# Kernel optimization log

Hardware: AMD Instinct MI355X
Metric: run time of the kernel (lower is better)

Reference implementation:

```python
import jax, jax.numpy as jnp
import numpy as np

DEPTH = 6

def sparsemax(z):
    # sparsemax over last axis (Martins & Astudillo 2016)
    z_sorted = -jnp.sort(-z, axis=-1)
    z_cum = jnp.cumsum(z_sorted, axis=-1)
    k = jnp.arange(1, z.shape[-1] + 1, dtype=z.dtype)
    support = k * z_sorted > z_cum - 1.0
    k_sup = jnp.sum(support, axis=-1, keepdims=True).astype(jnp.int32)
    tau_sum = jnp.take_along_axis(z_cum, k_sup - 1, axis=-1)
    tau = (tau_sum - 1.0) / k_sup.astype(z.dtype)
    return jnp.maximum(z - tau, 0.0)

def sparsemoid(x):
    return jnp.clip(0.5 * x + 0.5, 0.0, 1.0)

def make_bin_codes(depth):
    indices = jnp.arange(2 ** depth)
    offsets = 2 ** jnp.arange(depth)
    bin_codes = ((indices[None, :] // offsets[:, None]) % 2).astype(jnp.float32)
    return jnp.stack([bin_codes, 1.0 - bin_codes], axis=-1)  # [depth, 2^depth, 2]

def odste_forward(x, fsl, esl, thr, lt, resp, codes):
    # x: [B,J,D]; fsl: [n,t,J]; esl: [n,t,J,D]; thr/lt: [n,t]; resp: [n,c,D,2^t]
    fs = sparsemax(fsl)                               # [n,t,J]
    es = sparsemax(esl)                               # [n,t,J,D]
    sel = jnp.einsum('bjd,ntj->bntd', x, fs)          # feature selection
    sel = sel * jnp.sum(es, axis=2)[None]             # einsum 'bntd,ntjd->bntd'
    tl = (sel - thr[None, :, :, None]) * jnp.exp(-lt)[None, :, :, None]
    tl = jnp.stack([-tl, tl], axis=-1)                # [b,n,t,d,2]
    bins = sparsemoid(tl)
    bm = jnp.einsum('bntds,tcs->bntdc', bins, codes)  # [b,n,t,d,c]
    rw = jnp.prod(bm, axis=2)                         # [b,n,d,c]
    return jnp.einsum('bnds,ncds->bnd', rw, resp)     # [b,n,d]


def setup_inputs() -> dict:
    key = jax.random.key(0)
    B, D, n, t, c_tree = 64, 32, 128, DEPTH, 1
    Js = [64, 192, 320]
    ks = jax.random.split(key, 1 + 5 * len(Js))
    inp = {'x': jax.random.normal(ks[0], (B, Js[0], D), dtype=jnp.float32)}
    for i, J in enumerate(Js):
        k0, k1, k2, k3, k4 = ks[1 + 5 * i:6 + 5 * i]
        inp[f'fsl_{i}'] = jax.random.uniform(k0, (n, t, J), dtype=jnp.float32)
        inp[f'esl_{i}'] = jax.random.normal(k1, (n, t, J, D), dtype=jnp.float32)
        inp[f'thr_{i}'] = jax.random.normal(k2, (n, t), dtype=jnp.float32)
        inp[f'lt_{i}'] = jax.random.normal(k3, (n, t), dtype=jnp.float32)
        inp[f'resp_{i}'] = jax.random.normal(k4, (n, c_tree, D, 2 ** t), dtype=jnp.float32)
    return inp


def reference(x, fsl_0, esl_0, thr_0, lt_0, resp_0,
              fsl_1, esl_1, thr_1, lt_1, resp_1,
              fsl_2, esl_2, thr_2, lt_2, resp_2):
    codes = make_bin_codes(DEPTH)
    layers = [(fsl_0, esl_0, thr_0, lt_0, resp_0),
              (fsl_1, esl_1, thr_1, lt_1, resp_1),
              (fsl_2, esl_2, thr_2, lt_2, resp_2)]
    for fsl, esl, thr, lt, resp in layers:
        h = odste_forward(x, fsl, esl, thr, lt, resp, codes)
        x = jnp.concatenate([x, h], axis=1)
    return x
```

## Files before the change

kernel.cpp:

```cpp
#include <hip/hip_runtime.h>

#define OUT_COLS 448
#define OUT_STRIDE (OUT_COLS * 32)
#define NTREES 128
#define TDEPTH 6
#define NT (NTREES * TDEPTH)
#define DD 32
#define BB 64
#define PADW 64

template <int CTRL, int RMASK = 0xf, bool BC = true>
__device__ __forceinline__ float dppf(float v) {
    return __int_as_float(
        __builtin_amdgcn_update_dpp(0, __float_as_int(v), CTRL, RMASK, 0xf, BC));
}

__device__ __forceinline__ float wred64(float x) {
    x += dppf<0x111>(x);
    x += dppf<0x112>(x);
    x += dppf<0x114>(x);
    x += dppf<0x118>(x);
    x += __int_as_float(__builtin_amdgcn_update_dpp(0, __float_as_int(x), 0x142, 0xa, 0xf, false));
    x += __int_as_float(__builtin_amdgcn_update_dpp(0, __float_as_int(x), 0x143, 0xc, 0xf, false));
    return __int_as_float(__builtin_amdgcn_readlane(__float_as_int(x), 63));
}

template <int J>
__device__ __forceinline__ void fs_row(const float* __restrict__ zr, int lane,
                                       float2* __restrict__ fjv, int* __restrict__ fcnt_p) {
    constexpr int T = J / 64;
    float z[T];
    #pragma unroll
    for (int t = 0; t < T; ++t) z[t] = zr[t * 64 + lane];
    float sp = 0.f;
    #pragma unroll
    for (int t = 0; t < T; ++t) sp += z[t];
    float k = (float)J;
    float tau = (wred64(sp) - 1.f) / k;
    #pragma unroll 1
    for (int it = 0; it < 64; ++it) {
        float s2 = 0.f, c2 = 0.f;
        #pragma unroll
        for (int t = 0; t < T; ++t) {
            bool g = z[t] > tau;
            s2 += g ? z[t] : 0.f;
            c2 += g ? 1.f : 0.f;
        }
        float S2 = wred64(s2);
        float K2 = wred64(c2);
        if (K2 == k) break;
        k = K2;
        tau = (S2 - 1.f) / K2;
    }
    unsigned long long below = (1ull << lane) - 1ull;
    int base = 0;
    #pragma unroll
    for (int t = 0; t < T; ++t) {
        bool sup = z[t] > tau;
        unsigned long long m = __ballot(sup);
        int pos = base + __popcll(m & below);
        if (sup && pos < PADW)
            fjv[pos] = make_float2(__int_as_float((t * 64 + lane) * 128), z[t] - tau);
        base += __popcll(m);
    }
    int cnt = base < PADW ? base : PADW;
    for (int i = cnt + lane; i < PADW; i += 64)
        fjv[i] = make_float2(__int_as_float(0), 0.f);
    if (lane == 0) *fcnt_p = cnt;
}

template <int S>
__device__ __forceinline__ void bstep(float* a, int lane) {
    constexpr int half = 16 >> S;
    bool up = ((lane >> S) & 1) != 0;
    #pragma unroll
    for (int q = 0; q < half; ++q) {
        float send = up ? a[q] : a[half + q];
        float recv;
        if constexpr (S == 0)      recv = dppf<0xB1>(send);
        else if constexpr (S == 1) recv = dppf<0x4E>(send);
        else recv = __int_as_float(__builtin_amdgcn_ds_swizzle(
                        __float_as_int(send), ((1 << S) << 10) | 0x1F));
        float keep = up ? a[half + q] : a[q];
        a[q] = keep + recv;
    }
}

__device__ __forceinline__ void es_task(int w, int lane,
                                        const float* __restrict__ e0,
                                        const float* __restrict__ e1,
                                        const float* __restrict__ e2,
                                        float* __restrict__ part) {
    const float* esl; int row, chunk, J; size_t grow;
    if (w < NT)          { esl = e0; row = w; chunk = 0; J = 64; grow = (size_t)row; }
    else if (w < 4 * NT) { int q = w - NT; esl = e1; row = q / 3; chunk = q - row * 3; J = 192; grow = (size_t)(NT + row); }
    else                 { int q = w - 4 * NT; esl = e2; row = q / 5; chunk = q - row * 5; J = 320; grow = (size_t)(2 * NT + row); }

    const float4* zp4 = (const float4*)(esl + ((size_t)row * J + chunk * 64 + lane) * 32);
    float z[32];
    #pragma unroll
    for (int i = 0; i < 8; ++i) {
        float4 v = zp4[i];
        z[4 * i] = v.x; z[4 * i + 1] = v.y; z[4 * i + 2] = v.z; z[4 * i + 3] = v.w;
    }
    float mx = z[0];
    #pragma unroll
    for (int i = 1; i < 32; ++i) mx = fmaxf(mx, z[i]);
    float tau = mx - 1.0f;
    int kprev = -1;
    #pragma unroll 1
    for (int it = 0; it < 40; ++it) {
        float s0 = 0.f, s1 = 0.f, s2 = 0.f, s3 = 0.f;
        int k0 = 0, k1 = 0, k2 = 0, k3 = 0;
        #pragma unroll
        for (int i = 0; i < 8; ++i) {
            bool g0 = z[4 * i]     > tau; s0 += g0 ? z[4 * i]     : 0.f; k0 += g0;
            bool g1 = z[4 * i + 1] > tau; s1 += g1 ? z[4 * i + 1] : 0.f; k1 += g1;
            bool g2 = z[4 * i + 2] > tau; s2 += g2 ? z[4 * i + 2] : 0.f; k2 += g2;
            bool g3 = z[4 * i + 3] > tau; s3 += g3 ? z[4 * i + 3] : 0.f; k3 += g3;
        }
        float S = (s0 + s1) + (s2 + s3);
        int k = (k0 + k1) + (k2 + k3);
        bool chg = (k != kprev);
        kprev = k;
        tau = (S - 1.0f) / (float)k;
        if (__ballot(chg) == 0ull) break;
    }
    #pragma unroll
    for (int i = 0; i < 32; ++i) z[i] = fmaxf(z[i] - tau, 0.f);
    bstep<0>(z, lane);
    bstep<1>(z, lane);
    bstep<2>(z, lane);
    bstep<3>(z, lane);
    bstep<4>(z, lane);
    z[0] += __shfl_xor(z[0], 32, 64);
    if (lane < 32) {
        int d = ((lane & 1) << 4) | ((lane & 2) << 2) | (lane & 4)
              | ((lane & 8) >> 2) | ((lane & 16) >> 4);
        part[(grow * 5 + chunk) * 32 + d] = z[0];
    }
}

__global__ __launch_bounds__(256)
void prep_kernel(const float* __restrict__ x,
                 const float* __restrict__ f0, const float* __restrict__ f1,
                 const float* __restrict__ f2,
                 const float* __restrict__ e0, const float* __restrict__ e1,
                 const float* __restrict__ e2,
                 float2* __restrict__ fjv, int* __restrict__ fcnt,
                 float* __restrict__ part, float* __restrict__ out, int esEnd) {
    int w = blockIdx.x * 4 + (threadIdx.x >> 6);
    int lane = threadIdx.x & 63;

    if (w < 512) {
        const float4* x4 = (const float4*)x;
        float4* o4 = (float4*)out;
        int g = w * 64 + lane;
        int b = g >> 9, r = g & 511;
        o4[(size_t)b * (OUT_STRIDE / 4) + r] = x4[g];
        return;
    }
    w -= 512;
    if (w < 3 * NT) {
        if (w < NT) {
            fs_row<64>(f0 + (size_t)w * 64, lane, fjv + (size_t)w * PADW, fcnt + w);
        } else if (w < 2 * NT) {
            int r = w - NT;
            fs_row<192>(f1 + (size_t)r * 192, lane,
                        fjv + (size_t)(NT + r) * PADW, fcnt + NT + r);
        } else {
            int r = w - 2 * NT;
            fs_row<320>(f2 + (size_t)r * 320, lane,
                        fjv + (size_t)(2 * NT + r) * PADW, fcnt + 2 * NT + r);
        }
        return;
    }
    w -= 3 * NT;
    if (w < esEnd) es_task(w, lane, e0, e1, e2, part);
}

__global__ __launch_bounds__(256)
void mainplus_kernel(const float2* __restrict__ fjvL, const int* __restrict__ fcnt,
                     const float* __restrict__ partL, int nch,
                     const float* __restrict__ thr, const float* __restrict__ lt,
                     const float* __restrict__ resp,
                     float* __restrict__ out, int colOff,
                     const float* __restrict__ e0, const float* __restrict__ e1,
                     const float* __restrict__ e2, float* __restrict__ partAll,
                     int nMain, int esBeg, int esEnd) {
    int tid = threadIdx.x;
    if ((int)blockIdx.x >= nMain) {
        int w = esBeg + (blockIdx.x - nMain) * 4 + (tid >> 6);
        if (w < esEnd) es_task(w, tid & 63, e0, e1, e2, partAll);
        return;
    }
    int n = blockIdx.x & (NTREES - 1);
    int by = blockIdx.x >> 7;
    __shared__ float4 s_jv[TDEPTH][PADW / 2];
    __shared__ float2 s_resp2[DD][33];
    __shared__ float  s_ess[TDEPTH][DD];
    __shared__ float  s_thr[TDEPTH], s_elt[TDEPTH];
    __shared__ int    s_cnt[TDEPTH];

    {
        const float4* g = (const float4*)(fjvL + (size_t)n * TDEPTH * PADW);
        if (tid < 192) ((float4*)s_jv)[tid] = g[tid];
    }
    {
        const float2* g = (const float2*)(resp + (size_t)n * (DD * 64));
        for (int i = tid; i < DD * 32; i += 256)
            s_resp2[i >> 5][i & 31] = g[i];
    }
    if (tid < TDEPTH * DD) {
        int t = tid >> 5, d = tid & 31;
        float e = 0.f;
        #pragma unroll
        for (int c = 0; c < 5; ++c)
            if (c < nch) e += partL[((size_t)(n * TDEPTH + t) * 5 + c) * 32 + d];
        s_ess[t][d] = e;
    }
    if (tid < TDEPTH) {
        int r = n * TDEPTH + tid;
        s_thr[tid] = thr[r];
        s_elt[tid] = expf(-lt[r]);
        s_cnt[tid] = fcnt[r];
    }
    __syncthreads();

    int b = by * 8 + (tid >> 5);
    int d = tid & 31;
    const char* xbd = (const char*)(out + (size_t)b * OUT_STRIDE + d);

    int maxc = s_cnt[0];
    #pragma unroll
    for (int t = 1; t < TDEPTH; ++t) maxc = max(maxc, s_cnt[t]);
    int rounds = (maxc + 7) >> 3;

    float acc0 = 0.f, acc1 = 0.f, acc2 = 0.f, acc3 = 0.f, acc4 = 0.f, acc5 = 0.f;
    for (int r = 0; r < rounds; ++r) {
        int p4 = r * 4;
        #pragma unroll
        for (int t = 0; t < TDEPTH; ++t) {
            float4 q0 = s_jv[t][p4 + 0];
            float4 q1 = s_jv[t][p4 + 1];
            float4 q2 = s_jv[t][p4 + 2];
            float4 q3 = s_jv[t][p4 + 3];
            float x0 = *(const float*)(xbd + __float_as_int(q0.x));
            float x1 = *(const float*)(xbd + __float_as_int(q0.z));
            float x2 = *(const float*)(xbd + __float_as_int(q1.x));
            float x3 = *(const float*)(xbd + __float_as_int(q1.z));
            float x4 = *(const float*)(xbd + __float_as_int(q2.x));
            float x5 = *(const float*)(xbd + __float_as_int(q2.z));
            float x6 = *(const float*)(xbd + __float_as_int(q3.x));
            float x7 = *(const float*)(xbd + __float_as_int(q3.z));
            float a = ((x0 * q0.y + x1 * q0.w) + (x2 * q1.y + x3 * q1.w))
                    + ((x4 * q2.y + x5 * q2.w) + (x6 * q3.y + x7 * q3.w));
            if (t == 0) acc0 += a;
            if (t == 1) acc1 += a;
            if (t == 2) acc2 += a;
            if (t == 3) acc3 += a;
            if (t == 4) acc4 += a;
            if (t == 5) acc5 += a;
        }
    }
    float sv[TDEPTH];
    {
        float accs[TDEPTH] = {acc0, acc1, acc2, acc3, acc4, acc5};
        #pragma unroll
        for (int t = 0; t < TDEPTH; ++t) {
            float sel = accs[t] * s_ess[t][d];
            float tlv = (sel - s_thr[t]) * s_elt[t];
            sv[t] = fminf(fmaxf(0.5f * tlv + 0.5f, 0.f), 1.f);
        }
    }

    float A[8], Bv[8];
    {
        float a0 = sv[0], a1 = 1.f - sv[0];
        float b0 = sv[1], b1 = 1.f - sv[1];
        float c0 = sv[2], c1 = 1.f - sv[2];
        A[0] = a0 * b0 * c0; A[1] = a1 * b0 * c0;
        A[2] = a0 * b1 * c0; A[3] = a1 * b1 * c0;
        A[4] = a0 * b0 * c1; A[5] = a1 * b0 * c1;
        A[6] = a0 * b1 * c1; A[7] = a1 * b1 * c1;
        float d0 = sv[3], d1 = 1.f - sv[3];
        float e0 = sv[4], e1 = 1.f - sv[4];
        float f0 = sv[5], f1 = 1.f - sv[5];
        Bv[0] = d0 * e0 * f0; Bv[1] = d1 * e0 * f0;
        Bv[2] = d0 * e1 * f0; Bv[3] = d1 * e1 * f0;
        Bv[4] = d0 * e0 * f1; Bv[5] = d1 * e0 * f1;
        Bv[6] = d0 * e1 * f1; Bv[7] = d1 * e1 * f1;
    }
    float o = 0.f;
    #pragma unroll
    for (int c2 = 0; c2 < 8; ++c2) {
        float2 r0 = s_resp2[d][(8 * c2) >> 1];
        float2 r1 = s_resp2[d][(8 * c2 + 2) >> 1];
        float2 r2 = s_resp2[d][(8 * c2 + 4) >> 1];
        float2 r3 = s_resp2[d][(8 * c2 + 6) >> 1];
        float inner = (A[0] * r0.x + A[1] * r0.y) + (A[2] * r1.x + A[3] * r1.y)
                    + (A[4] * r2.x + A[5] * r2.y) + (A[6] * r3.x + A[7] * r3.y);
        o += Bv[c2] * inner;
    }
    out[(size_t)b * OUT_STRIDE + (size_t)(colOff + n) * DD + d] = o;
}

extern "C" void kernel_launch(void* const* d_in, const int* in_sizes, int n_in,
                              void* d_out, int out_size, void* d_ws, size_t ws_size,
                              hipStream_t stream) {
    const float* x = (const float*)d_in[0];
    float* out = (float*)d_out;

    const size_t NPAD = (size_t)3 * NT * PADW;
    char* ws = (char*)d_ws;
    float2* fjv  = (float2*)(ws);
    int*    fcnt = (int*)(ws + NPAD * 8);
    float*  part = (float*)(ws + NPAD * 8 + 16384);

    const float* e0 = (const float*)d_in[2];
    const float* e1 = (const float*)d_in[7];
    const float* e2 = (const float*)d_in[12];

    const int ES_A = 2304;
    const int ES_B = 4608;

    prep_kernel<<<5120 / 4, 256, 0, stream>>>(
        x,
        (const float*)d_in[1], (const float*)d_in[6], (const float*)d_in[11],
        e0, e1, e2, fjv, fcnt, part, out, ES_A);

    const int nchs[3] = {1, 3, 5};
    int colOff = 64;
    for (int L = 0; L < 3; ++L) {
        const float* thr  = (const float*)d_in[3 + 5 * L];
        const float* lt   = (const float*)d_in[4 + 5 * L];
        const float* resp = (const float*)d_in[5 + 5 * L];
        int esBeg = (L == 0) ? ES_A : (L == 1) ? ES_B : 0;
        int esEnd = (L == 0) ? ES_B : (L == 1) ? 6912 : 0;
        int nEsBlocks = (esEnd - esBeg + 3) / 4;
        mainplus_kernel<<<1024 + nEsBlocks, 256, 0, stream>>>(
            fjv + (size_t)L * NT * PADW, fcnt + L * NT,
            part + (size_t)L * NT * 5 * 32, nchs[L],
            thr, lt, resp, out, colOff,
            e0, e1, e2, part, 1024, esBeg, esEnd);
        colOff += NTREES;
    }
}
```

Measured before the change: 59.22 us.

## Gather x rows as float4 per lane with support split across lane groups

Restructures the sparse feature-selection gather. Each thread previously loaded scalar x values for its own d over 8 support entries per round. Now each lane loads float4 slices of 4 consecutive d values, the support entries are spread over 4 lane groups, and partial sums are combined with shuffle reductions before each lane picks its d. This is meant to cut the number of memory instructions and widen each access, at the cost of extra shuffles and a lane-to-d remapping.

```diff
diff --git a/kernel.cpp b/kernel.cpp
--- a/kernel.cpp
+++ b/kernel.cpp
@@ -179,6 +179,24 @@
     if (w < esEnd) es_task(w, lane, e0, e1, e2, part);
 }
 
+#define GATHER_T(sjvt, acc) {                                            \
+    float4 q = (sjvt)[qi];                                               \
+    float4 xA = *(const float4*)(xb16 + __float_as_int(q.x));            \
+    float4 xB = *(const float4*)(xb16 + __float_as_int(q.z));            \
+    acc.x = fmaf(xA.x, q.y, fmaf(xB.x, q.w, acc.x));                     \
+    acc.y = fmaf(xA.y, q.y, fmaf(xB.y, q.w, acc.y));                     \
+    acc.z = fmaf(xA.z, q.y, fmaf(xB.z, q.w, acc.z));                     \
+    acc.w = fmaf(xA.w, q.y, fmaf(xB.w, q.w, acc.w)); }
+
+#define REDSTEP(a, M) { a.x += __shfl_xor(a.x, M); a.y += __shfl_xor(a.y, M); \
+                        a.z += __shfl_xor(a.z, M); a.w += __shfl_xor(a.w, M); }
+
+__device__ __forceinline__ float selr(float4 v, int r) {
+    float lo = (r & 1) ? v.y : v.x;
+    float hi = (r & 1) ? v.w : v.z;
+    return (r & 2) ? hi : lo;
+}
+
 __global__ __launch_bounds__(256)
 void mainplus_kernel(const float2* __restrict__ fjvL, const int* __restrict__ fcnt,
                      const float* __restrict__ partL, int nch,
@@ -227,45 +245,40 @@
     }
     __syncthreads();
 
-    int b = by * 8 + (tid >> 5);
-    int d = tid & 31;
-    const char* xbd = (const char*)(out + (size_t)b * OUT_STRIDE + d);
+    int b   = by * 8 + (tid >> 5);
+    int sub = tid & 31;
+    int r   = sub >> 3;
+    int dq  = sub & 7;
+    const char* xb16 = (const char*)(out + (size_t)b * OUT_STRIDE) + dq * 16;
 
     int maxc = s_cnt[0];
     #pragma unroll
     for (int t = 1; t < TDEPTH; ++t) maxc = max(maxc, s_cnt[t]);
     int rounds = (maxc + 7) >> 3;
 
-    float acc0 = 0.f, acc1 = 0.f, acc2 = 0.f, acc3 = 0.f, acc4 = 0.f, acc5 = 0.f;
-    for (int r = 0; r < rounds; ++r) {
-        int p4 = r * 4;
-        #pragma unroll
-        for (int t = 0; t < TDEPTH; ++t) {
-            float4 q0 = s_jv[t][p4 + 0];
-            float4 q1 = s_jv[t][p4 + 1];
-            float4 q2 = s_jv[t][p4 + 2];
-            float4 q3 = s_jv[t][p4 + 3];
-            float x0 = *(const float*)(xbd + __float_as_int(q0.x));
-            float x1 = *(const float*)(xbd + __float_as_int(q0.z));
-            float x2 = *(const float*)(xbd + __float_as_int(q1.x));
-            float x3 = *(const float*)(xbd + __float_as_int(q1.z));
-            float x4 = *(const float*)(xbd + __float_as_int(q2.x));
-            float x5 = *(const float*)(xbd + __float_as_int(q2.z));
-            float x6 = *(const float*)(xbd + __float_as_int(q3.x));
-            float x7 = *(const float*)(xbd + __float_as_int(q3.z));
-            float a = ((x0 * q0.y + x1 * q0.w) + (x2 * q1.y + x3 * q1.w))
-                    + ((x4 * q2.y + x5 * q2.w) + (x6 * q3.y + x7 * q3.w));
-            if (t == 0) acc0 += a;
-            if (t == 1) acc1 += a;
-            if (t == 2) acc2 += a;
-            if (t == 3) acc3 += a;
-            if (t == 4) acc4 += a;
-            if (t == 5) acc5 += a;
-        }
-    }
+    float4 a0 = {0,0,0,0}, a1 = {0,0,0,0}, a2 = {0,0,0,0};
+    float4 a3 = {0,0,0,0}, a4 = {0,0,0,0}, a5 = {0,0,0,0};
+    for (int m = 0; m < rounds; ++m) {
+        int qi = r + 4 * m;
+        GATHER_T(s_jv[0], a0);
+        GATHER_T(s_jv[1], a1);
+        GATHER_T(s_jv[2], a2);
+        GATHER_T(s_jv[3], a3);
+        GATHER_T(s_jv[4], a4);
+        GATHER_T(s_jv[5], a5);
+    }
+    REDSTEP(a0, 8);  REDSTEP(a0, 16);
+    REDSTEP(a1, 8);  REDSTEP(a1, 16);
+    REDSTEP(a2, 8);  REDSTEP(a2, 16);
+    REDSTEP(a3, 8);  REDSTEP(a3, 16);
+    REDSTEP(a4, 8);  REDSTEP(a4, 16);
+    REDSTEP(a5, 8);  REDSTEP(a5, 16);
+
+    int d = 4 * dq + r;
     float sv[TDEPTH];
     {
-        float accs[TDEPTH] = {acc0, acc1, acc2, acc3, acc4, acc5};
+        float accs[TDEPTH] = { selr(a0, r), selr(a1, r), selr(a2, r),
+                               selr(a3, r), selr(a4, r), selr(a5, r) };
         #pragma unroll
         for (int t = 0; t < TDEPTH; ++t) {
             float sel = accs[t] * s_ess[t][d];
@@ -276,20 +289,20 @@
 
     float A[8], Bv[8];
     {
-        float a0 = sv[0], a1 = 1.f - sv[0];
-        float b0 = sv[1], b1 = 1.f - sv[1];
+        float p0 = sv[0], p1 = 1.f - sv[0];
+        float q0 = sv[1], q1 = 1.f - sv[1];
         float c0 = sv[2], c1 = 1.f - sv[2];
-        A[0] = a0 * b0 * c0; A[1] = a1 * b0 * c0;
-        A[2] = a0 * b1 * c0; A[3] = a1 * b1 * c0;
-        A[4] = a0 * b0 * c1; A[5] = a1 * b0 * c1;
-        A[6] = a0 * b1 * c1; A[7] = a1 * b1 * c1;
-        float d0 = sv[3], d1 = 1.f - sv[3];
-        float e0 = sv[4], e1 = 1.f - sv[4];
-        float f0 = sv[5], f1 = 1.f - sv[5];
-        Bv[0] = d0 * e0 * f0; Bv[1] = d1 * e0 * f0;
-        Bv[2] = d0 * e1 * f0; Bv[3] = d1 * e1 * f0;
-        Bv[4] = d0 * e0 * f1; Bv[5] = d1 * e0 * f1;
-        Bv[6] = d0 * e1 * f1; Bv[7] = d1 * e1 * f1;
+        A[0] = p0 * q0 * c0; A[1] = p1 * q0 * c0;
+        A[2] = p0 * q1 * c0; A[3] = p1 * q1 * c0;
+        A[4] = p0 * q0 * c1; A[5] = p1 * q0 * c1;
+        A[6] = p0 * q1 * c1; A[7] = p1 * q1 * c1;
+        float u0 = sv[3], u1 = 1.f - sv[3];
+        float v0 = sv[4], v1 = 1.f - sv[4];
+        float w0 = sv[5], w1 = 1.f - sv[5];
+        Bv[0] = u0 * v0 * w0; Bv[1] = u1 * v0 * w0;
+        Bv[2] = u0 * v1 * w0; Bv[3] = u1 * v1 * w0;
+        Bv[4] = u0 * v0 * w1; Bv[5] = u1 * v0 * w1;
+        Bv[6] = u0 * v1 * w1; Bv[7] = u1 * v1 * w1;
     }
     float o = 0.f;
     #pragma unroll
```

Result: slower. 60.66 us (+2.4%).
